# Kernel optimization log

Measured on AMD Instinct MI355X. Metric: run time of the kernel, lower is better.

Reference implementation:

```python
import jax, jax.numpy as jnp
import numpy as np

B, S, D = 2, 2048, 1024
H, HD = 16, 64

def setup_inputs() -> dict:
    key = jax.random.key(0)
    k1, k2, k3, k4 = jax.random.split(key, 4)
    inputs = jax.random.normal(k1, (B, S, D), dtype=jnp.float32)
    scale = 1.0 / np.sqrt(D)
    Wq = jax.random.normal(k2, (D, H * HD), dtype=jnp.float32) * scale
    Wk = jax.random.normal(k3, (D, H * HD), dtype=jnp.float32) * scale
    Wv = jax.random.normal(k4, (D, H * HD), dtype=jnp.float32) * scale
    return {"inputs": inputs, "Wq": Wq, "Wk": Wk, "Wv": Wv}

def _split_heads(x):
    # [B,S,H*HD] -> [B,H,S,HD]; tf.split along last axis == reshape then transpose
    b, s, _ = x.shape
    return x.reshape(b, s, H, HD).transpose(0, 2, 1, 3)

def reference(inputs, Wq, Wk, Wv):
    q = _split_heads(inputs @ Wq)  # [B,H,S,HD]
    k = _split_heads(inputs @ Wk)
    v = _split_heads(inputs @ Wv)
    scores = jnp.einsum("bhsd,bhtd->bhst", q, k) / jnp.sqrt(jnp.float32(HD))
    attn = jax.nn.softmax(scores, axis=-1)  # [B,H,S,S]
    out = jnp.einsum("bhst,bhtd->bhsd", attn, v)  # [B,H,S,HD]
    # concat heads back: [B,S,H*HD]
    return out.transpose(0, 2, 1, 3).reshape(inputs.shape[0], inputs.shape[1], H * HD)
```

## Files before the change

kernel.cpp:

```cpp
#include <hip/hip_runtime.h>

typedef __attribute__((ext_vector_type(8))) short short8;
typedef __attribute__((ext_vector_type(4))) float f32x4;
typedef __attribute__((ext_vector_type(16))) float f32x16;

#define B_  2
#define S_  2048
#define D_  1024
#define H_  16
#define HD_ 64
#define M_  (B_*S_)
#define N_  (H_*HD_)
#define HSZ ((size_t)B_*H_*S_*HD_)
#define BHS_ (B_*H_*S_)

#define QSCALE 0.18033688011112042f

__device__ __forceinline__ unsigned short f2bf(float f) {
  unsigned int u = __float_as_uint(f);
  u += 0x7fffu + ((u >> 16) & 1u);
  return (unsigned short)(u >> 16);
}

__device__ __forceinline__ unsigned int cvt_pk_bf16(float lo, float hi) {
  unsigned int r;
  asm("v_cvt_pk_bf16_f32 %0, %1, %2" : "=v"(r) : "v"(lo), "v"(hi));
  return r;
}

__device__ __forceinline__ float exp2_fast(float x) {
  float r;
  asm("v_exp_f32 %0, %1" : "=v"(r) : "v"(x));
  return r;
}

__device__ __forceinline__ void gll16(const void* g, void* l) {
  __builtin_amdgcn_global_load_lds(
      (const __attribute__((address_space(1))) void*)g,
      (__attribute__((address_space(3))) void*)l, 16, 0, 0);
}

__global__ void cvt_x_kernel(const float* __restrict__ x, unsigned short* __restrict__ xb) {
  int i = blockIdx.x * blockDim.x + threadIdx.x;
  float4 v = reinterpret_cast<const float4*>(x)[i];
  ushort4 o;
  o.x = f2bf(v.x); o.y = f2bf(v.y); o.z = f2bf(v.z); o.w = f2bf(v.w);
  reinterpret_cast<ushort4*>(xb)[i] = o;
}

__global__ void cvt_w_transpose_kernel(const float* __restrict__ w0, const float* __restrict__ w1,
                                       const float* __restrict__ w2, unsigned short* __restrict__ wt) {
  __shared__ float tile[32][33];
  const float* w = blockIdx.z == 0 ? w0 : (blockIdx.z == 1 ? w1 : w2);
  unsigned short* o = wt + (size_t)blockIdx.z * D_ * N_;
  int kbase = blockIdx.y * 32, nbase = blockIdx.x * 32;
#pragma unroll
  for (int i = 0; i < 4; i++)
    tile[threadIdx.y + i*8][threadIdx.x] =
        w[(size_t)(kbase + threadIdx.y + i*8) * N_ + nbase + threadIdx.x];
  __syncthreads();
#pragma unroll
  for (int i = 0; i < 4; i++)
    o[(size_t)(nbase + threadIdx.y + i*8) * D_ + kbase + threadIdx.x] =
        f2bf(tile[threadIdx.x][threadIdx.y + i*8]);
}

__global__ __launch_bounds__(256) void qkv_gemm_kernel(const unsigned short* __restrict__ xb,
                                                       const unsigned short* __restrict__ wt,
                                                       unsigned short* __restrict__ qkv) {
  __shared__ __align__(16) unsigned short As[128 * 64];
  __shared__ __align__(16) unsigned short Bs[128 * 64];
  const unsigned short* w = wt + (size_t)blockIdx.z * D_ * N_;
  unsigned short* out = qkv + (size_t)blockIdx.z * HSZ;
  int lane = threadIdx.x & 63, wave = threadIdx.x >> 6;
  int lr = lane & 15, lk = lane >> 4;
  int mblk = blockIdx.y * 128, nblk = blockIdx.x * 128;
  int wm = (wave >> 1) * 64, wn = (wave & 1) * 64;

  int srow0 = wave * 32 + (lane >> 3);
  int scol = lane & 7;
  f32x4 acc[4][4] = {};

  for (int kk = 0; kk < D_; kk += 64) {
    __syncthreads();
#pragma unroll
    for (int it = 0; it < 4; it++) {
      int row = srow0 + it * 8;
      int ce = (scol ^ (row & 7)) * 8;
      gll16(xb + (size_t)(mblk + row) * D_ + kk + ce,
            (void*)(As + (size_t)(wave * 4 + it) * 512));
      gll16(w  + (size_t)(nblk + row) * D_ + kk + ce,
            (void*)(Bs + (size_t)(wave * 4 + it) * 512));
    }
    __syncthreads();

    short8 a[2][4], b[2][4];
#pragma unroll
    for (int i = 0; i < 4; i++) {
      int row = wm + i * 16 + lr;
      const char* rp = (const char*)As + row * 128;
#pragma unroll
      for (int ks = 0; ks < 2; ks++)
        a[ks][i] = *reinterpret_cast<const short8*>(rp + ((((ks*4 + lk) ^ (row & 7))) << 4));
    }
#pragma unroll
    for (int j = 0; j < 4; j++) {
      int row = wn + j * 16 + lr;
      const char* rp = (const char*)Bs + row * 128;
#pragma unroll
      for (int ks = 0; ks < 2; ks++)
        b[ks][j] = *reinterpret_cast<const short8*>(rp + ((((ks*4 + lk) ^ (row & 7))) << 4));
    }
#pragma unroll
    for (int ks = 0; ks < 2; ks++)
#pragma unroll
      for (int i = 0; i < 4; i++)
#pragma unroll
        for (int j = 0; j < 4; j++)
          acc[i][j] = __builtin_amdgcn_mfma_f32_16x16x32_bf16(a[ks][i], b[ks][j], acc[i][j], 0, 0, 0);
  }

  if (blockIdx.z == 2) {
#pragma unroll
    for (int i = 0; i < 4; i++) {
      int m0 = mblk + wm + i*16 + lk*4;
      int bb = m0 >> 11, s0 = m0 & (S_-1);
#pragma unroll
      for (int j = 0; j < 4; j++) {
        int n = nblk + wn + j*16 + lr;
        int h = n >> 6, d = n & (HD_-1);
        ushort4 pk;
        pk.x = f2bf(acc[i][j][0]); pk.y = f2bf(acc[i][j][1]);
        pk.z = f2bf(acc[i][j][2]); pk.w = f2bf(acc[i][j][3]);
        *reinterpret_cast<ushort4*>(out + ((size_t)(bb*H_ + h)*HD_ + d)*S_ + s0) = pk;
      }
    }
  } else {
    float qs = (blockIdx.z == 0) ? QSCALE : 1.0f;
#pragma unroll
    for (int i = 0; i < 4; i++)
#pragma unroll
      for (int j = 0; j < 4; j++)
#pragma unroll
        for (int r = 0; r < 4; r++) {
          int m = mblk + wm + i*16 + lk*4 + r;
          int n = nblk + wn + j*16 + lr;
          int bb = m >> 11, s = m & (S_-1), h = n >> 6, d = n & (HD_-1);
          out[(((size_t)bb * H_ + h) * S_ + s) * HD_ + d] = f2bf(acc[i][j][r] * qs);
        }
  }
}

__global__ __launch_bounds__(256, 4) void attn_kernel(const unsigned short* __restrict__ qkv,
                                                      float* __restrict__ Opart,
                                                      float* __restrict__ ML) {
  int hid = blockIdx.x;
  int wrk = (hid & 7) * 128 + (hid >> 3);
  int bh = wrk >> 5, qtile = (wrk >> 1) & 15, half = wrk & 1;

  const unsigned short* Q  = qkv +            (size_t)bh * S_ * HD_;
  const unsigned short* K  = qkv + HSZ   +    (size_t)bh * S_ * HD_;
  const unsigned short* Vt = qkv + 2*HSZ +    (size_t)bh * HD_ * S_;
  int lane = threadIdx.x & 63, wave = threadIdx.x >> 6;
  int ql = lane & 31, hi = lane >> 5;
  int qbase = qtile * 128 + wave * 32;
  int tid = threadIdx.x;
  int kv0 = half * (S_/2);

  __shared__ __align__(16) unsigned short Ks[2][64 * 64];
  __shared__ __align__(16) unsigned short Vs[2][64 * 64];

#define STAGE(b, kc) do {                                                        \
    _Pragma("unroll")                                                            \
    for (int it = 0; it < 2; it++) {                                             \
      int ci = it * 256 + tid;                                                   \
      int rr = ci >> 3, cc = ci & 7;                                             \
      int ce = (cc ^ (rr & 7) ^ ((rr >> 3) & 7)) * 8;                            \
      gll16(K  + (size_t)((kc) + rr) * HD_ + ce, (void*)(Ks[b] + (size_t)ci*8)); \
      gll16(Vt + (size_t)rr * S_ + (kc) + ce,    (void*)(Vs[b] + (size_t)ci*8)); \
    }                                                                            \
  } while (0)

  short8 qf[4];
#pragma unroll
  for (int ds = 0; ds < 4; ds++)
    qf[ds] = *reinterpret_cast<const short8*>(Q + (size_t)(qbase + ql) * HD_ + ds*16 + hi*8);

  short8 ones;
#pragma unroll
  for (int i = 0; i < 8; i++) ones[i] = (short)0x3F80;

  f32x16 oacc[2] = {};
  f32x16 lacc = {};
  float m = -INFINITY;

  STAGE(0, kv0);

  int buf = 0;
  for (int kt = 0; kt < S_/128; kt++) {
    __syncthreads();
    if (kt < S_/128 - 1) STAGE(buf^1, kv0 + (kt+1)*64);

    f32x16 sacc[2] = {};
    __builtin_amdgcn_s_setprio(1);
#pragma unroll
    for (int kh = 0; kh < 2; kh++) {
      int row = kh*32 + ql;
      const char* rp = (const char*)Ks[buf] + row * 128;
      int sw = (row & 7) ^ ((row >> 3) & 7);
#pragma unroll
      for (int ds = 0; ds < 4; ds++) {
        short8 kf = *reinterpret_cast<const short8*>(rp + (((ds*2 + hi) ^ sw) << 4));
        sacc[kh] = __builtin_amdgcn_mfma_f32_32x32x16_bf16(kf, qf[ds], sacc[kh], 0, 0, 0);
      }
    }
    __builtin_amdgcn_s_setprio(0);

    float tm[16];
#pragma unroll
    for (int r = 0; r < 16; r++) tm[r] = fmaxf(sacc[0][r], sacc[1][r]);
#pragma unroll
    for (int st = 8; st > 0; st >>= 1)
#pragma unroll
      for (int r = 0; r < st; r++) tm[r] = fmaxf(tm[r], tm[r + st]);
    float mx = fmaxf(tm[0], __shfl_xor(tm[0], 32));
    if (__any(mx - m > 8.0f)) {
      float mnew = fmaxf(m, mx);
      float corr = exp2_fast(m - mnew);
      m = mnew;
      lacc[0] *= corr;
#pragma unroll
      for (int dh = 0; dh < 2; dh++)
#pragma unroll
        for (int r = 0; r < 16; r++) oacc[dh][r] *= corr;
    }
#pragma unroll
    for (int kh = 0; kh < 2; kh++)
#pragma unroll
      for (int r = 0; r < 16; r++)
        sacc[kh][r] = exp2_fast(sacc[kh][r] - m);

#pragma unroll
    for (int ks = 0; ks < 4; ks++) {
      int o = (ks & 1) * 8;
      int kh = ks >> 1;
      unsigned int w0 = cvt_pk_bf16(sacc[kh][o+0], sacc[kh][o+1]);
      unsigned int w1 = cvt_pk_bf16(sacc[kh][o+2], sacc[kh][o+3]);
      unsigned int w2 = cvt_pk_bf16(sacc[kh][o+4], sacc[kh][o+5]);
      unsigned int w3 = cvt_pk_bf16(sacc[kh][o+6], sacc[kh][o+7]);
      asm("v_permlane32_swap_b32 %0, %1" : "+v"(w0), "+v"(w2));
      asm("v_permlane32_swap_b32 %0, %1" : "+v"(w1), "+v"(w3));
      union { unsigned int u[4]; short8 s; } pf;
      pf.u[0] = w0; pf.u[1] = w1; pf.u[2] = w2; pf.u[3] = w3;
      __builtin_amdgcn_s_setprio(1);
      lacc = __builtin_amdgcn_mfma_f32_32x32x16_bf16(ones, pf.s, lacc, 0, 0, 0);
#pragma unroll
      for (int dh = 0; dh < 2; dh++) {
        int row = dh*32 + ql;
        int sw = (row & 7) ^ ((row >> 3) & 7);
        short8 vf = *reinterpret_cast<const short8*>(
            (const char*)Vs[buf] + row * 128 + (((ks*2 + hi) ^ sw) << 4));
        oacc[dh] = __builtin_amdgcn_mfma_f32_32x32x16_bf16(vf, pf.s, oacc[dh], 0, 0, 0);
      }
      __builtin_amdgcn_s_setprio(0);
    }
    buf ^= 1;
  }

  int s = qbase + ql;
  size_t prow = (size_t)half * BHS_ + (size_t)bh * S_ + s;
  float* orow = Opart + prow * HD_;
#pragma unroll
  for (int dh = 0; dh < 2; dh++)
#pragma unroll
    for (int a = 0; a < 4; a++) {
      float4 vv;
      vv.x = oacc[dh][a*4+0]; vv.y = oacc[dh][a*4+1];
      vv.z = oacc[dh][a*4+2]; vv.w = oacc[dh][a*4+3];
      *reinterpret_cast<float4*>(orow + dh*32 + 8*a + 4*hi) = vv;
    }
  if (hi == 0) {
    float2 ml; ml.x = m; ml.y = lacc[0];
    reinterpret_cast<float2*>(ML)[prow] = ml;
  }
#undef STAGE
}

__global__ __launch_bounds__(256) void combine_kernel(const float* __restrict__ Opart,
                                                      const float* __restrict__ ML,
                                                      float* __restrict__ out) {
  int idx = blockIdx.x * 256 + threadIdx.x;
  int row = idx >> 4;
  int dc = (idx & 15) * 4;
  float2 ml0 = reinterpret_cast<const float2*>(ML)[row];
  float2 ml1 = reinterpret_cast<const float2*>(ML)[BHS_ + row];
  float M = fmaxf(ml0.x, ml1.x);
  float w0 = exp2_fast(ml0.x - M), w1 = exp2_fast(ml1.x - M);
  float inv = 1.0f / (ml0.y * w0 + ml1.y * w1);
  float4 o0 = *reinterpret_cast<const float4*>(Opart + (size_t)row * HD_ + dc);
  float4 o1 = *reinterpret_cast<const float4*>(Opart + ((size_t)BHS_ + row) * HD_ + dc);
  float4 r;
  r.x = (o0.x*w0 + o1.x*w1) * inv; r.y = (o0.y*w0 + o1.y*w1) * inv;
  r.z = (o0.z*w0 + o1.z*w1) * inv; r.w = (o0.w*w0 + o1.w*w1) * inv;
  int bh = row >> 11, s = row & (S_-1);
  int b = bh >> 4, h = bh & (H_-1);
  *reinterpret_cast<float4*>(out + ((size_t)b * S_ + s) * N_ + h * HD_ + dc) = r;
}

extern "C" void kernel_launch(void* const* d_in, const int* in_sizes, int n_in,
                              void* d_out, int out_size, void* d_ws, size_t ws_size,
                              hipStream_t stream) {
  const float* X  = (const float*)d_in[0];
  const float* Wq = (const float*)d_in[1];
  const float* Wk = (const float*)d_in[2];
  const float* Wv = (const float*)d_in[3];
  float* out = (float*)d_out;

  unsigned short* Xb  = (unsigned short*)d_ws;
  unsigned short* Wt  = Xb + (size_t)M_ * D_;
  unsigned short* QKV = Wt + (size_t)3 * D_ * N_;
  float* Opart = (float*)(QKV + 3 * HSZ);
  float* ML    = Opart + (size_t)2 * BHS_ * HD_;

  cvt_x_kernel<<<(M_*D_)/(256*4), 256, 0, stream>>>(X, Xb);
  cvt_w_transpose_kernel<<<dim3(N_/32, D_/32, 3), dim3(32, 8), 0, stream>>>(Wq, Wk, Wv, Wt);
  qkv_gemm_kernel<<<dim3(N_/128, M_/128, 3), 256, 0, stream>>>(Xb, Wt, QKV);
  attn_kernel<<<(S_/128) * (B_*H_) * 2, 256, 0, stream>>>(QKV, Opart, ML);
  combine_kernel<<<(BHS_*16)/256, 256, 0, stream>>>(Opart, ML, out);
}
```

Measured before the change: 129.6 us.

## Process two 32-row Q tiles per wave to reuse K/V fragments

Each wave now handles 64 query rows (two 32-row sub-tiles) instead of 32, so K and V fragments loaded from LDS are reused across two MFMA streams. The grid shrinks to half the blocks, with 256 query rows per block. The row-sum MFMA uses split ones masks so a single lacc accumulator carries both sub-tiles' sums. This lowers LDS traffic and staging per query, but raises register pressure (launch bounds relaxed to 2) and halves block count, which may reduce occupancy and latency hiding.

```diff
diff --git a/kernel.cpp b/kernel.cpp
--- a/kernel.cpp
+++ b/kernel.cpp
@@ -151,19 +151,19 @@
   }
 }
 
-__global__ __launch_bounds__(256, 4) void attn_kernel(const unsigned short* __restrict__ qkv,
+__global__ __launch_bounds__(256, 2) void attn_kernel(const unsigned short* __restrict__ qkv,
                                                       float* __restrict__ Opart,
                                                       float* __restrict__ ML) {
   int hid = blockIdx.x;
-  int wrk = (hid & 7) * 128 + (hid >> 3);
-  int bh = wrk >> 5, qtile = (wrk >> 1) & 15, half = wrk & 1;
+  int wrk = (hid & 7) * 64 + (hid >> 3);
+  int bh = wrk >> 4, qt2 = (wrk >> 1) & 7, half = wrk & 1;
 
   const unsigned short* Q  = qkv +            (size_t)bh * S_ * HD_;
   const unsigned short* K  = qkv + HSZ   +    (size_t)bh * S_ * HD_;
   const unsigned short* Vt = qkv + 2*HSZ +    (size_t)bh * HD_ * S_;
   int lane = threadIdx.x & 63, wave = threadIdx.x >> 6;
   int ql = lane & 31, hi = lane >> 5;
-  int qbase = qtile * 128 + wave * 32;
+  int qbase = qt2 * 256 + wave * 64;
   int tid = threadIdx.x;
   int kv0 = half * (S_/2);
 
@@ -181,107 +181,168 @@
     }                                                                            \
   } while (0)
 
-  short8 qf[4];
-#pragma unroll
-  for (int ds = 0; ds < 4; ds++)
-    qf[ds] = *reinterpret_cast<const short8*>(Q + (size_t)(qbase + ql) * HD_ + ds*16 + hi*8);
-
-  short8 ones;
-#pragma unroll
-  for (int i = 0; i < 8; i++) ones[i] = (short)0x3F80;
-
-  f32x16 oacc[2] = {};
+  short8 qf[2][4];
+#pragma unroll
+  for (int qt = 0; qt < 2; qt++)
+#pragma unroll
+    for (int ds = 0; ds < 4; ds++)
+      qf[qt][ds] = *reinterpret_cast<const short8*>(
+          Q + (size_t)(qbase + qt*32 + ql) * HD_ + ds*16 + hi*8);
+
+  unsigned short o0v = (ql < 16) ? 0x3F80 : 0;
+  short8 ones0, ones1;
+#pragma unroll
+  for (int i = 0; i < 8; i++) { ones0[i] = (short)o0v; ones1[i] = (short)(o0v ^ 0x3F80); }
+
+  f32x16 oacc[2][2] = {};
   f32x16 lacc = {};
-  float m = -INFINITY;
+  float m0 = -INFINITY, m1 = -INFINITY;
 
   STAGE(0, kv0);
 
-  int buf = 0;
+#pragma unroll 2
   for (int kt = 0; kt < S_/128; kt++) {
+    int buf = kt & 1;
     __syncthreads();
     if (kt < S_/128 - 1) STAGE(buf^1, kv0 + (kt+1)*64);
 
-    f32x16 sacc[2] = {};
-    __builtin_amdgcn_s_setprio(1);
+    short8 kf[2][4];
 #pragma unroll
     for (int kh = 0; kh < 2; kh++) {
       int row = kh*32 + ql;
       const char* rp = (const char*)Ks[buf] + row * 128;
       int sw = (row & 7) ^ ((row >> 3) & 7);
 #pragma unroll
+      for (int ds = 0; ds < 4; ds++)
+        kf[kh][ds] = *reinterpret_cast<const short8*>(rp + (((ds*2 + hi) ^ sw) << 4));
+    }
+    f32x16 s0[2] = {}, s1[2] = {};
+    __builtin_amdgcn_s_setprio(1);
+#pragma unroll
+    for (int kh = 0; kh < 2; kh++)
+#pragma unroll
       for (int ds = 0; ds < 4; ds++) {
-        short8 kf = *reinterpret_cast<const short8*>(rp + (((ds*2 + hi) ^ sw) << 4));
-        sacc[kh] = __builtin_amdgcn_mfma_f32_32x32x16_bf16(kf, qf[ds], sacc[kh], 0, 0, 0);
-      }
-    }
+        s0[kh] = __builtin_amdgcn_mfma_f32_32x32x16_bf16(kf[kh][ds], qf[0][ds], s0[kh], 0, 0, 0);
+        s1[kh] = __builtin_amdgcn_mfma_f32_32x32x16_bf16(kf[kh][ds], qf[1][ds], s1[kh], 0, 0, 0);
+      }
     __builtin_amdgcn_s_setprio(0);
 
-    float tm[16];
-#pragma unroll
-    for (int r = 0; r < 16; r++) tm[r] = fmaxf(sacc[0][r], sacc[1][r]);
-#pragma unroll
-    for (int st = 8; st > 0; st >>= 1)
-#pragma unroll
-      for (int r = 0; r < st; r++) tm[r] = fmaxf(tm[r], tm[r + st]);
-    float mx = fmaxf(tm[0], __shfl_xor(tm[0], 32));
-    if (__any(mx - m > 8.0f)) {
-      float mnew = fmaxf(m, mx);
-      float corr = exp2_fast(m - mnew);
-      m = mnew;
-      lacc[0] *= corr;
-#pragma unroll
-      for (int dh = 0; dh < 2; dh++)
-#pragma unroll
-        for (int r = 0; r < 16; r++) oacc[dh][r] *= corr;
-    }
-#pragma unroll
-    for (int kh = 0; kh < 2; kh++)
-#pragma unroll
-      for (int r = 0; r < 16; r++)
-        sacc[kh][r] = exp2_fast(sacc[kh][r] - m);
-
+    {
+      float tm[16];
+#pragma unroll
+      for (int r = 0; r < 16; r++) tm[r] = fmaxf(s0[0][r], s0[1][r]);
+#pragma unroll
+      for (int st = 8; st > 0; st >>= 1)
+#pragma unroll
+        for (int r = 0; r < st; r++) tm[r] = fmaxf(tm[r], tm[r + st]);
+      float mx = fmaxf(tm[0], __shfl_xor(tm[0], 32));
+      if (__any(mx - m0 > 8.0f)) {
+        float mn = fmaxf(m0, mx);
+        float c = exp2_fast(m0 - mn);
+        m0 = mn;
+#pragma unroll
+        for (int r = 0; r < 8; r++) lacc[r] *= c;
+#pragma unroll
+        for (int dh = 0; dh < 2; dh++)
+#pragma unroll
+          for (int r = 0; r < 16; r++) oacc[0][dh][r] *= c;
+      }
+#pragma unroll
+      for (int kh = 0; kh < 2; kh++)
+#pragma unroll
+        for (int r = 0; r < 16; r++) s0[kh][r] = exp2_fast(s0[kh][r] - m0);
+    }
+    {
+      float tm[16];
+#pragma unroll
+      for (int r = 0; r < 16; r++) tm[r] = fmaxf(s1[0][r], s1[1][r]);
+#pragma unroll
+      for (int st = 8; st > 0; st >>= 1)
+#pragma unroll
+        for (int r = 0; r < st; r++) tm[r] = fmaxf(tm[r], tm[r + st]);
+      float mx = fmaxf(tm[0], __shfl_xor(tm[0], 32));
+      if (__any(mx - m1 > 8.0f)) {
+        float mn = fmaxf(m1, mx);
+        float c = exp2_fast(m1 - mn);
+        m1 = mn;
+#pragma unroll
+        for (int r = 8; r < 16; r++) lacc[r] *= c;
+#pragma unroll
+        for (int dh = 0; dh < 2; dh++)
+#pragma unroll
+          for (int r = 0; r < 16; r++) oacc[1][dh][r] *= c;
+      }
+#pragma unroll
+      for (int kh = 0; kh < 2; kh++)
+#pragma unroll
+        for (int r = 0; r < 16; r++) s1[kh][r] = exp2_fast(s1[kh][r] - m1);
+    }
+
+    short8 vf[4][2];
 #pragma unroll
     for (int ks = 0; ks < 4; ks++) {
       int o = (ks & 1) * 8;
       int kh = ks >> 1;
-      unsigned int w0 = cvt_pk_bf16(sacc[kh][o+0], sacc[kh][o+1]);
-      unsigned int w1 = cvt_pk_bf16(sacc[kh][o+2], sacc[kh][o+3]);
-      unsigned int w2 = cvt_pk_bf16(sacc[kh][o+4], sacc[kh][o+5]);
-      unsigned int w3 = cvt_pk_bf16(sacc[kh][o+6], sacc[kh][o+7]);
+      unsigned int w0 = cvt_pk_bf16(s0[kh][o+0], s0[kh][o+1]);
+      unsigned int w1 = cvt_pk_bf16(s0[kh][o+2], s0[kh][o+3]);
+      unsigned int w2 = cvt_pk_bf16(s0[kh][o+4], s0[kh][o+5]);
+      unsigned int w3 = cvt_pk_bf16(s0[kh][o+6], s0[kh][o+7]);
       asm("v_permlane32_swap_b32 %0, %1" : "+v"(w0), "+v"(w2));
       asm("v_permlane32_swap_b32 %0, %1" : "+v"(w1), "+v"(w3));
-      union { unsigned int u[4]; short8 s; } pf;
+      union { unsigned int u[4]; short8 v; } pf;
       pf.u[0] = w0; pf.u[1] = w1; pf.u[2] = w2; pf.u[3] = w3;
       __builtin_amdgcn_s_setprio(1);
-      lacc = __builtin_amdgcn_mfma_f32_32x32x16_bf16(ones, pf.s, lacc, 0, 0, 0);
+      lacc = __builtin_amdgcn_mfma_f32_32x32x16_bf16(ones0, pf.v, lacc, 0, 0, 0);
 #pragma unroll
       for (int dh = 0; dh < 2; dh++) {
         int row = dh*32 + ql;
         int sw = (row & 7) ^ ((row >> 3) & 7);
-        short8 vf = *reinterpret_cast<const short8*>(
+        vf[ks][dh] = *reinterpret_cast<const short8*>(
             (const char*)Vs[buf] + row * 128 + (((ks*2 + hi) ^ sw) << 4));
-        oacc[dh] = __builtin_amdgcn_mfma_f32_32x32x16_bf16(vf, pf.s, oacc[dh], 0, 0, 0);
+        oacc[0][dh] = __builtin_amdgcn_mfma_f32_32x32x16_bf16(vf[ks][dh], pf.v, oacc[0][dh], 0, 0, 0);
       }
       __builtin_amdgcn_s_setprio(0);
     }
-    buf ^= 1;
+#pragma unroll
+    for (int ks = 0; ks < 4; ks++) {
+      int o = (ks & 1) * 8;
+      int kh = ks >> 1;
+      unsigned int w0 = cvt_pk_bf16(s1[kh][o+0], s1[kh][o+1]);
+      unsigned int w1 = cvt_pk_bf16(s1[kh][o+2], s1[kh][o+3]);
+      unsigned int w2 = cvt_pk_bf16(s1[kh][o+4], s1[kh][o+5]);
+      unsigned int w3 = cvt_pk_bf16(s1[kh][o+6], s1[kh][o+7]);
+      asm("v_permlane32_swap_b32 %0, %1" : "+v"(w0), "+v"(w2));
+      asm("v_permlane32_swap_b32 %0, %1" : "+v"(w1), "+v"(w3));
+      union { unsigned int u[4]; short8 v; } pf;
+      pf.u[0] = w0; pf.u[1] = w1; pf.u[2] = w2; pf.u[3] = w3;
+      __builtin_amdgcn_s_setprio(1);
+      lacc = __builtin_amdgcn_mfma_f32_32x32x16_bf16(ones1, pf.v, lacc, 0, 0, 0);
+#pragma unroll
+      for (int dh = 0; dh < 2; dh++)
+        oacc[1][dh] = __builtin_amdgcn_mfma_f32_32x32x16_bf16(vf[ks][dh], pf.v, oacc[1][dh], 0, 0, 0);
+      __builtin_amdgcn_s_setprio(0);
+    }
   }
 
-  int s = qbase + ql;
-  size_t prow = (size_t)half * BHS_ + (size_t)bh * S_ + s;
-  float* orow = Opart + prow * HD_;
-#pragma unroll
-  for (int dh = 0; dh < 2; dh++)
-#pragma unroll
-    for (int a = 0; a < 4; a++) {
-      float4 vv;
-      vv.x = oacc[dh][a*4+0]; vv.y = oacc[dh][a*4+1];
-      vv.z = oacc[dh][a*4+2]; vv.w = oacc[dh][a*4+3];
-      *reinterpret_cast<float4*>(orow + dh*32 + 8*a + 4*hi) = vv;
-    }
-  if (hi == 0) {
-    float2 ml; ml.x = m; ml.y = lacc[0];
-    reinterpret_cast<float2*>(ML)[prow] = ml;
+#pragma unroll
+  for (int qt = 0; qt < 2; qt++) {
+    float l = lacc[qt * 8];
+    int s = qbase + qt*32 + ql;
+    size_t prow = (size_t)half * BHS_ + (size_t)bh * S_ + s;
+    float* orow = Opart + prow * HD_;
+#pragma unroll
+    for (int dh = 0; dh < 2; dh++)
+#pragma unroll
+      for (int a = 0; a < 4; a++) {
+        float4 vv;
+        vv.x = oacc[qt][dh][a*4+0]; vv.y = oacc[qt][dh][a*4+1];
+        vv.z = oacc[qt][dh][a*4+2]; vv.w = oacc[qt][dh][a*4+3];
+        *reinterpret_cast<float4*>(orow + dh*32 + 8*a + 4*hi) = vv;
+      }
+    if (hi == 0) {
+      float2 ml; ml.x = (qt == 0) ? m0 : m1; ml.y = l;
+      reinterpret_cast<float2*>(ML)[prow] = ml;
+    }
   }
 #undef STAGE
 }
@@ -325,6 +386,6 @@
   cvt_x_kernel<<<(M_*D_)/(256*4), 256, 0, stream>>>(X, Xb);
   cvt_w_transpose_kernel<<<dim3(N_/32, D_/32, 3), dim3(32, 8), 0, stream>>>(Wq, Wk, Wv, Wt);
   qkv_gemm_kernel<<<dim3(N_/128, M_/128, 3), 256, 0, stream>>>(Xb, Wt, QKV);
-  attn_kernel<<<(S_/128) * (B_*H_) * 2, 256, 0, stream>>>(QKV, Opart, ML);
+  attn_kernel<<<(S_/256) * (B_*H_) * 2, 256, 0, stream>>>(QKV, Opart, ML);
   combine_kernel<<<(BHS_*16)/256, 256, 0, stream>>>(Opart, ML, out);
 }
```

Measured after the change: 122.1 us. 1.06x faster.
